# Performance work log

Hardware: AMD Instinct MI355X
Metric: run time of the kernel (lower is better)

The kernel has to match this reference:

```python
import jax, jax.numpy as jnp
import numpy as np

B, S, D, H = 1, 2048, 1024, 16
DH = D // H  # 64
ROPE_THETA = 10000.0


def _rope_tables(seq_len, half_dim, theta):
    inv = 1.0 / (theta ** (np.arange(0, half_dim, dtype=np.float32) / half_dim))
    ang = np.arange(seq_len, dtype=np.float32)[:, None] * inv[None, :]
    return jnp.asarray(np.cos(ang)), jnp.asarray(np.sin(ang))


def setup_inputs() -> dict:
    key = jax.random.key(0)
    ks = jax.random.split(key, 6)
    x = jax.random.normal(ks[0], (B, S, D), dtype=jnp.float32)
    # block-diagonal mask over ~4 packed images -> sorted segment ids
    seg_ids = jnp.sort(jax.random.randint(ks[1], (S,), 0, 4, dtype=jnp.int32))
    freqs_cos, freqs_sin = _rope_tables(S, DH // 2, ROPE_THETA)
    scale = 1.0 / np.sqrt(D)
    wq = jax.random.normal(ks[2], (D, D), dtype=jnp.float32) * scale
    wk = jax.random.normal(ks[3], (D, D), dtype=jnp.float32) * scale
    wv = jax.random.normal(ks[4], (D, D), dtype=jnp.float32) * scale
    wo = jax.random.normal(ks[5], (D, D), dtype=jnp.float32) * scale
    return {"x": x, "seg_ids": seg_ids, "freqs_cos": freqs_cos,
            "freqs_sin": freqs_sin, "wq": wq, "wk": wk, "wv": wv, "wo": wo}


def _apply_rope(t, cos, sin):
    # t: [B,S,H,DH]; interpret last dim as DH//2 complex pairs (real, imag)
    tr = t.reshape(B, S, H, DH // 2, 2)
    a, b = tr[..., 0], tr[..., 1]
    c = cos[None, :, None, :]  # [1,S,1,DH/2]
    s = sin[None, :, None, :]
    out = jnp.stack([a * c - b * s, a * s + b * c], axis=-1)
    return out.reshape(B, S, H, DH)


def reference(x, seg_ids, freqs_cos, freqs_sin, wq, wk, wv, wo):
    q = (x @ wq.T).reshape(B, S, H, DH)
    k = (x @ wk.T).reshape(B, S, H, DH)
    v = (x @ wv.T).reshape(B, S, H, DH)
    q = _apply_rope(q, freqs_cos, freqs_sin)
    k = _apply_rope(k, freqs_cos, freqs_sin)
    scores = jnp.einsum('bqhd,bkhd->bhqk', q, k) / np.float32(np.sqrt(DH))
    block_mask = (seg_ids[:, None] == seg_ids[None, :])  # [S,S] block-diagonal
    scores = jnp.where(block_mask[None, None], scores, jnp.float32(-1e9))
    attn = jax.nn.softmax(scores, axis=-1)
    out = jnp.einsum('bhqk,bkhd->bqhd', attn, v).reshape(B, S, D)
    return out @ wo.T
```

## Files before the change

### kernel.cpp

```cpp
#include <hip/hip_runtime.h>

typedef __bf16 bf16;
typedef __bf16 bf16x4 __attribute__((ext_vector_type(4)));
typedef __bf16 bf16x8 __attribute__((ext_vector_type(8)));
typedef float  f32x4  __attribute__((ext_vector_type(4)));

#define S_LEN 2048
#define D_DIM 1024
#define NHEAD 16
#define DHEAD 64

__device__ __forceinline__ void async_cp16(const bf16* g, bf16* l) {
  __builtin_amdgcn_global_load_lds(
      (__attribute__((address_space(1))) void*)(void*)g,
      (__attribute__((address_space(3))) void*)l,
      16, 0, 0);
}

__global__ __launch_bounds__(256) void cvt_k(
    const float* __restrict__ x,  const float* __restrict__ w0,
    const float* __restrict__ w1, const float* __restrict__ w2,
    const float* __restrict__ w3, bf16* __restrict__ dst,
    const int* __restrict__ seg, int* __restrict__ kbr)
{
  __shared__ int firstv[4];
  const int b = blockIdx.x;
  const int t = threadIdx.x;

  if (b < 3072) {
    int i = b * 256 + t;
    const float* src;
    int off;
    if (i < (1 << 18)) {
      src = x; off = i;
    } else {
      int j = i - (1 << 18);
      int s = j >> 17;
      off = j & ((1 << 17) - 1);
      src = (s == 0) ? w0 : (s == 1) ? w1 : (s == 2) ? w2 : w3;
    }
    f32x4 a = *(const f32x4*)(src + (size_t)off * 8);
    f32x4 bb = *(const f32x4*)(src + (size_t)off * 8 + 4);
    bf16x8 o;
    o[0] = (bf16)a[0];  o[1] = (bf16)a[1];  o[2] = (bf16)a[2];  o[3] = (bf16)a[3];
    o[4] = (bf16)bb[0]; o[5] = (bf16)bb[1]; o[6] = (bf16)bb[2]; o[7] = (bf16)bb[3];
    *((bf16x8*)dst + i) = o;
  } else {
    if (t < 4) firstv[t] = S_LEN;
    __syncthreads();
    for (int i = t; i < S_LEN; i += 256) {
      int s = seg[i];
      if (i == 0 || seg[i - 1] != s) atomicMin(&firstv[s], i);
    }
    __syncthreads();
    if (t < 32) {
      int smin = seg[t * 64], smax = seg[t * 64 + 63];
      int lb = S_LEN, ub = S_LEN;
      for (int vv = smin; vv < 4; ++vv) lb = min(lb, firstv[vv]);
      for (int vv = smax + 1; vv < 4; ++vv) ub = min(ub, firstv[vv]);
      kbr[t * 2] = lb >> 6;
      kbr[t * 2 + 1] = (ub - 1) >> 6;
    }
  }
}

__global__ __launch_bounds__(256) void gemm_qkv(
    const bf16* __restrict__ A,
    const bf16* __restrict__ B0, const bf16* __restrict__ B1,
    const bf16* __restrict__ B2,
    const float* __restrict__ cosT, const float* __restrict__ sinT,
    bf16* __restrict__ Cbase, bf16* __restrict__ Vt)
{
  constexpr int K = 1024, N = 1024;
  const int z = blockIdx.z;
  const bf16* W = (z == 0) ? B0 : (z == 1) ? B1 : B2;
  bf16* C = Cbase + (size_t)z * 2048 * 1024;

  __shared__ bf16 As0[128 * 32] __attribute__((aligned(16)));
  __shared__ bf16 As1[128 * 32] __attribute__((aligned(16)));
  __shared__ bf16 Bs0[64 * 32] __attribute__((aligned(16)));
  __shared__ bf16 Bs1[64 * 32] __attribute__((aligned(16)));

  const int t = threadIdx.x;
  const int lane = t & 63;
  const int w = t >> 6;
  const int lm = lane & 15, lq = lane >> 4;
  const int wr = w >> 1, wc = w & 1;
  const int bm = blockIdx.y, bn = blockIdx.x;

  const bf16* Abase = A + (size_t)bm * 128 * K;
  const bf16* Wbase = W + (size_t)bn * 64 * K;

  f32x4 acc[4][2] = {};

  for (int kk = 0; kk < K; kk += 64) {
#pragma unroll
    for (int g = 0; g < 2; ++g) {
      int c = (w * 2 + g) * 64 + lane;
      int row = c >> 2, k8 = c & 3;
      const bf16* ga = Abase + (size_t)row * K + kk + k8 * 8;
      async_cp16(ga, As0 + (w * 2 + g) * 512);
      async_cp16(ga + 32, As1 + (w * 2 + g) * 512);
    }
    {
      int c = w * 64 + lane;
      int row = c >> 2, k8 = c & 3;
      const bf16* gb = Wbase + (size_t)row * K + kk + k8 * 8;
      async_cp16(gb, Bs0 + w * 512);
      async_cp16(gb + 32, Bs1 + w * 512);
    }
    __syncthreads();

#pragma unroll
    for (int ks = 0; ks < 2; ++ks) {
      const bf16* As = ks ? As1 : As0;
      const bf16* Bs = ks ? Bs1 : Bs0;
      bf16x8 af[4], bfr[2];
#pragma unroll
      for (int mi = 0; mi < 4; ++mi)
        af[mi] = *(const bf16x8*)&As[(wr * 64 + mi * 16 + lm) * 32 + lq * 8];
#pragma unroll
      for (int ni = 0; ni < 2; ++ni)
        bfr[ni] = *(const bf16x8*)&Bs[(wc * 32 + ni * 16 + lm) * 32 + lq * 8];
#pragma unroll
      for (int mi = 0; mi < 4; ++mi)
#pragma unroll
        for (int ni = 0; ni < 2; ++ni)
          acc[mi][ni] = __builtin_amdgcn_mfma_f32_16x16x32_bf16(
              af[mi], bfr[ni], acc[mi][ni], 0, 0, 0);
    }
    __syncthreads();
  }

  if (z < 2) {
    const float scale = (z == 0) ? 0.125f : 1.0f;
#pragma unroll
    for (int mi = 0; mi < 4; ++mi)
#pragma unroll
      for (int ni = 0; ni < 2; ++ni) {
        int gcol = bn * 64 + wc * 32 + ni * 16 + lm;
        int p = (gcol & 63) >> 1;
        bool even = (gcol & 1) == 0;
#pragma unroll
        for (int r = 0; r < 4; ++r) {
          int row = bm * 128 + wr * 64 + mi * 16 + lq * 4 + r;
          float v = acc[mi][ni][r];
          float mate = __shfl_xor(v, 1);
          float cv = cosT[row * 32 + p];
          float sv = sinT[row * 32 + p];
          float res = even ? (v * cv - mate * sv) : (mate * sv + v * cv);
          C[(size_t)row * N + gcol] = (bf16)(res * scale);
        }
      }
  } else {
#pragma unroll
    for (int mi = 0; mi < 4; ++mi)
#pragma unroll
      for (int ni = 0; ni < 2; ++ni) {
        int gcol = bn * 64 + wc * 32 + ni * 16 + lm;
        int rowb = bm * 128 + wr * 64 + mi * 16 + lq * 4;
        bf16x4 pack;
#pragma unroll
        for (int r = 0; r < 4; ++r) pack[r] = (bf16)acc[mi][ni][r];
        *(bf16x4*)(Vt + (size_t)gcol * S_LEN + rowb) = pack;
      }
  }
}

__global__ __launch_bounds__(256) void gemm_wo(
    const bf16* __restrict__ A, const bf16* __restrict__ W,
    float* __restrict__ C)
{
  constexpr int K = 1024, N = 1024;

  __shared__ bf16 As0[64 * 32] __attribute__((aligned(16)));
  __shared__ bf16 As1[64 * 32] __attribute__((aligned(16)));
  __shared__ bf16 Bs0[64 * 32] __attribute__((aligned(16)));
  __shared__ bf16 Bs1[64 * 32] __attribute__((aligned(16)));

  const int t = threadIdx.x;
  const int lane = t & 63;
  const int w = t >> 6;
  const int lm = lane & 15, lq = lane >> 4;
  const int bn = blockIdx.x, bm = blockIdx.y;

  const bf16* Abase = A + (size_t)bm * 64 * K;
  const bf16* Wbase = W + (size_t)bn * 64 * K;

  f32x4 acc[4] = {};

  for (int kk = 0; kk < K; kk += 64) {
    {
      int c = w * 64 + lane;
      int row = c >> 2, k8 = c & 3;
      const bf16* ga = Abase + (size_t)row * K + kk + k8 * 8;
      async_cp16(ga, As0 + w * 512);
      async_cp16(ga + 32, As1 + w * 512);
      const bf16* gb = Wbase + (size_t)row * K + kk + k8 * 8;
      async_cp16(gb, Bs0 + w * 512);
      async_cp16(gb + 32, Bs1 + w * 512);
    }
    __syncthreads();

#pragma unroll
    for (int ks = 0; ks < 2; ++ks) {
      const bf16* As = ks ? As1 : As0;
      const bf16* Bs = ks ? Bs1 : Bs0;
      bf16x8 af = *(const bf16x8*)&As[(w * 16 + lm) * 32 + lq * 8];
      bf16x8 bfr[4];
#pragma unroll
      for (int ni = 0; ni < 4; ++ni)
        bfr[ni] = *(const bf16x8*)&Bs[(ni * 16 + lm) * 32 + lq * 8];
#pragma unroll
      for (int ni = 0; ni < 4; ++ni)
        acc[ni] = __builtin_amdgcn_mfma_f32_16x16x32_bf16(
            af, bfr[ni], acc[ni], 0, 0, 0);
    }
    __syncthreads();
  }

#pragma unroll
  for (int ni = 0; ni < 4; ++ni) {
    int col = bn * 64 + ni * 16 + lm;
#pragma unroll
    for (int r = 0; r < 4; ++r) {
      int row = bm * 64 + w * 16 + lq * 4 + r;
      C[(size_t)row * N + col] = acc[ni][r];
    }
  }
}

__global__ __launch_bounds__(256) void attn_k(
    const bf16* __restrict__ Q, const bf16* __restrict__ Kmat,
    const bf16* __restrict__ Vt, const int* __restrict__ seg,
    const int* __restrict__ kbr,
    float* __restrict__ Opar, float* __restrict__ Lpar)
{
  __shared__ bf16 Ks[64 * 72] __attribute__((aligned(16)));
  __shared__ bf16 Vs[64 * 72] __attribute__((aligned(16)));
  __shared__ bf16 Ps[4][16 * 72] __attribute__((aligned(16)));
  __shared__ int segk[64];

  const int h = blockIdx.y;
  const int qt = blockIdx.x & 31, par = blockIdx.x >> 5;
  const int q0 = qt * 64;
  const int t = threadIdx.x, lane = t & 63, w = t >> 6;
  const int lm = lane & 15, lq = lane >> 4;
  const int qrow = q0 + w * 16;

  const int kb0f = kbr[qt * 2], kb1f = kbr[qt * 2 + 1];

  bf16x8 qf[2];
#pragma unroll
  for (int ks = 0; ks < 2; ++ks)
    qf[ks] = *(const bf16x8*)(Q + (size_t)(qrow + lm) * D_DIM + h * DHEAD +
                              ks * 32 + lq * 8);

  int sq[4];
  float l_i[4];
#pragma unroll
  for (int r = 0; r < 4; ++r) {
    sq[r] = seg[qrow + lq * 4 + r];
    l_i[r] = 0.0f;
  }
  f32x4 o[4] = {};

  const int srow0 = t >> 3, sch = (t & 7) * 8;
  const int srow1 = (256 + t) >> 3;

  const int kbS = kb0f + par;
  f32x4 pk0, pk1, pv0, pv1;
  int psg;
  if (kbS <= kb1f) {
    const int k0 = kbS * 64;
    pk0 = *(const f32x4*)(Kmat + (size_t)(k0 + srow0) * D_DIM + h * DHEAD + sch);
    pk1 = *(const f32x4*)(Kmat + (size_t)(k0 + srow1) * D_DIM + h * DHEAD + sch);
    pv0 = *(const f32x4*)(Vt + (size_t)(h * DHEAD + srow0) * S_LEN + k0 + sch);
    pv1 = *(const f32x4*)(Vt + (size_t)(h * DHEAD + srow1) * S_LEN + k0 + sch);
    if (t < 64) psg = seg[k0 + t];
  }

  for (int kb = kbS; kb <= kb1f; kb += 2) {
    __syncthreads();
    *(f32x4*)&Ks[srow0 * 72 + sch] = pk0;
    *(f32x4*)&Ks[srow1 * 72 + sch] = pk1;
    *(f32x4*)&Vs[srow0 * 72 + sch] = pv0;
    *(f32x4*)&Vs[srow1 * 72 + sch] = pv1;
    if (t < 64) segk[t] = psg;
    __syncthreads();

    if (kb + 2 <= kb1f) {
      const int k0 = (kb + 2) * 64;
      pk0 = *(const f32x4*)(Kmat + (size_t)(k0 + srow0) * D_DIM + h * DHEAD + sch);
      pk1 = *(const f32x4*)(Kmat + (size_t)(k0 + srow1) * D_DIM + h * DHEAD + sch);
      pv0 = *(const f32x4*)(Vt + (size_t)(h * DHEAD + srow0) * S_LEN + k0 + sch);
      pv1 = *(const f32x4*)(Vt + (size_t)(h * DHEAD + srow1) * S_LEN + k0 + sch);
      if (t < 64) psg = seg[k0 + t];
    }

    f32x4 sa[4] = {};
#pragma unroll
    for (int ks = 0; ks < 2; ++ks) {
      bf16x8 kf[4];
#pragma unroll
      for (int ni = 0; ni < 4; ++ni)
        kf[ni] = *(const bf16x8*)&Ks[(ni * 16 + lm) * 72 + ks * 32 + lq * 8];
#pragma unroll
      for (int ni = 0; ni < 4; ++ni)
        sa[ni] = __builtin_amdgcn_mfma_f32_16x16x32_bf16(qf[ks], kf[ni],
                                                         sa[ni], 0, 0, 0);
    }

    int sk[4];
#pragma unroll
    for (int ni = 0; ni < 4; ++ni) sk[ni] = segk[ni * 16 + lm];

#pragma unroll
    for (int r = 0; r < 4; ++r)
#pragma unroll
      for (int ni = 0; ni < 4; ++ni) {
        float p = (sq[r] == sk[ni]) ? __expf(sa[ni][r]) : 0.0f;
        l_i[r] += p;
        Ps[w][(lq * 4 + r) * 72 + ni * 16 + lm] = (bf16)p;
      }

#pragma unroll
    for (int ks = 0; ks < 2; ++ks) {
      bf16x8 pf = *(const bf16x8*)&Ps[w][lm * 72 + ks * 32 + lq * 8];
      bf16x8 vf[4];
#pragma unroll
      for (int ni = 0; ni < 4; ++ni)
        vf[ni] = *(const bf16x8*)&Vs[(ni * 16 + lm) * 72 + ks * 32 + lq * 8];
#pragma unroll
      for (int ni = 0; ni < 4; ++ni)
        o[ni] = __builtin_amdgcn_mfma_f32_16x16x32_bf16(pf, vf[ni], o[ni],
                                                        0, 0, 0);
    }
  }

  float* Ob = Opar + ((size_t)(par * NHEAD + h) * S_LEN) * DHEAD;
  float* Lb = Lpar + (size_t)(par * NHEAD + h) * S_LEN;
#pragma unroll
  for (int r = 0; r < 4; ++r) {
    float l = l_i[r];
    l += __shfl_xor(l, 1);
    l += __shfl_xor(l, 2);
    l += __shfl_xor(l, 4);
    l += __shfl_xor(l, 8);
    int row = qrow + lq * 4 + r;
    if (lm == 0) Lb[row] = l;
#pragma unroll
    for (int ni = 0; ni < 4; ++ni)
      Ob[(size_t)row * DHEAD + ni * 16 + lm] = o[ni][r];
  }
}

__global__ __launch_bounds__(256) void combine_k(
    const float* __restrict__ Opar, const float* __restrict__ Lpar,
    bf16* __restrict__ AO)
{
  int idx = blockIdx.x * 256 + threadIdx.x;
  int c4 = idx & 15;
  int rh = idx >> 4;
  int row = rh & 2047;
  int h = rh >> 11;
  const size_t PO = (size_t)NHEAD * S_LEN * DHEAD;
  const float* o0 = Opar + ((size_t)h * S_LEN + row) * DHEAD + c4 * 4;
  f32x4 a = *(const f32x4*)o0;
  f32x4 b = *(const f32x4*)(o0 + PO);
  float l = Lpar[(size_t)h * S_LEN + row] +
            Lpar[(size_t)NHEAD * S_LEN + (size_t)h * S_LEN + row];
  float inv = 1.0f / l;
  bf16x4 ov;
#pragma unroll
  for (int j = 0; j < 4; ++j) ov[j] = (bf16)((a[j] + b[j]) * inv);
  *(bf16x4*)(AO + (size_t)row * D_DIM + h * DHEAD + c4 * 4) = ov;
}

extern "C" void kernel_launch(void* const* d_in, const int* in_sizes, int n_in,
                              void* d_out, int out_size, void* d_ws,
                              size_t ws_size, hipStream_t stream)
{
  const float* x  = (const float*)d_in[0];
  const int*   sg = (const int*)d_in[1];
  const float* fc = (const float*)d_in[2];
  const float* fs = (const float*)d_in[3];
  const float* wq = (const float*)d_in[4];
  const float* wk = (const float*)d_in[5];
  const float* wv = (const float*)d_in[6];
  const float* wo = (const float*)d_in[7];
  float* out = (float*)d_out;

  const size_t MAT = (size_t)S_LEN * D_DIM;
  const size_t WSZ = (size_t)D_DIM * D_DIM;
  bf16* xb  = (bf16*)d_ws;
  bf16* wqb = xb + MAT;
  bf16* wkb = wqb + WSZ;
  bf16* wvb = wkb + WSZ;
  bf16* wob = wvb + WSZ;
  bf16* q0  = wob + WSZ;
  bf16* k0  = q0 + MAT;
  bf16* vt  = k0 + MAT;
  bf16* ao  = vt + MAT;
  float* opar = (float*)(ao + MAT);
  float* lpar = opar + 2 * MAT;
  int*   kbr  = (int*)(lpar + 2 * NHEAD * S_LEN);

  dim3 blk(256);
  cvt_k<<<dim3(3073), blk, 0, stream>>>(x, wq, wk, wv, wo, xb, sg, kbr);
  gemm_qkv<<<dim3(16, 16, 3), blk, 0, stream>>>(xb, wqb, wkb, wvb, fc, fs,
                                                q0, vt);
  attn_k<<<dim3(64, 16), blk, 0, stream>>>(q0, k0, vt, sg, kbr, opar, lpar);
  combine_k<<<dim3(2048), blk, 0, stream>>>(opar, lpar, ao);
  gemm_wo<<<dim3(16, 32), blk, 0, stream>>>(ao, wob, out);
}
```

Baseline: 148.8 us.

## Fuse split-attention combine into output projection and register-prefetch GEMM tiles

Removes the separate combine kernel: the Wo GEMM now reads the two fp32 partial attention outputs and normalizers directly, sums them, normalizes and converts to bf16 while staging its A tile into LDS. Both GEMMs also replace direct global-to-LDS async copies with register-staged prefetch of the next K tile, issued after the LDS write so the loads overlap the MFMA work. This saves one launch and the bf16 round trip through global memory. In exchange the Wo GEMM reads fp32 partials redundantly across all 16 column blocks, which is more traffic, and register pressure goes up.

```diff
diff --git a/kernel.cpp b/kernel.cpp
--- a/kernel.cpp
+++ b/kernel.cpp
@@ -9,13 +9,6 @@
 #define D_DIM 1024
 #define NHEAD 16
 #define DHEAD 64
-
-__device__ __forceinline__ void async_cp16(const bf16* g, bf16* l) {
-  __builtin_amdgcn_global_load_lds(
-      (__attribute__((address_space(1))) void*)(void*)g,
-      (__attribute__((address_space(3))) void*)l,
-      16, 0, 0);
-}
 
 __global__ __launch_bounds__(256) void cvt_k(
     const float* __restrict__ x,  const float* __restrict__ w0,
@@ -88,28 +81,45 @@
   const int wr = w >> 1, wc = w & 1;
   const int bm = blockIdx.y, bn = blockIdx.x;
 
-  const bf16* Abase = A + (size_t)bm * 128 * K;
-  const bf16* Wbase = W + (size_t)bn * 64 * K;
+  const int arow = t >> 3;
+  const int half = (t & 7) >> 2, off = (t & 3) * 8;
+  const int koff = half * 32 + off;
+  bf16* const Adst = (half ? As1 : As0);
+  bf16* const Bdst = (half ? Bs1 : Bs0);
+
+  const bf16* Abase = A + (size_t)bm * 128 * K + koff;
+  const bf16* Wbase = W + (size_t)bn * 64 * K + koff;
+
+  bf16x8 ra[4], rb[2];
+#pragma unroll
+  for (int i = 0; i < 4; ++i)
+    ra[i] = *(const bf16x8*)(Abase + (size_t)(arow + 32 * i) * K);
+#pragma unroll
+  for (int i = 0; i < 2; ++i)
+    rb[i] = *(const bf16x8*)(Wbase + (size_t)(arow + 32 * i) * K);
 
   f32x4 acc[4][2] = {};
 
   for (int kk = 0; kk < K; kk += 64) {
-#pragma unroll
-    for (int g = 0; g < 2; ++g) {
-      int c = (w * 2 + g) * 64 + lane;
-      int row = c >> 2, k8 = c & 3;
-      const bf16* ga = Abase + (size_t)row * K + kk + k8 * 8;
-      async_cp16(ga, As0 + (w * 2 + g) * 512);
-      async_cp16(ga + 32, As1 + (w * 2 + g) * 512);
-    }
-    {
-      int c = w * 64 + lane;
-      int row = c >> 2, k8 = c & 3;
-      const bf16* gb = Wbase + (size_t)row * K + kk + k8 * 8;
-      async_cp16(gb, Bs0 + w * 512);
-      async_cp16(gb + 32, Bs1 + w * 512);
-    }
-    __syncthreads();
+    __syncthreads();
+#pragma unroll
+    for (int i = 0; i < 4; ++i)
+      *(bf16x8*)&Adst[(arow + 32 * i) * 32 + off] = ra[i];
+#pragma unroll
+    for (int i = 0; i < 2; ++i)
+      *(bf16x8*)&Bdst[(arow + 32 * i) * 32 + off] = rb[i];
+    __syncthreads();
+
+    if (kk + 64 < K) {
+      const bf16* An = Abase + kk + 64;
+      const bf16* Wn = Wbase + kk + 64;
+#pragma unroll
+      for (int i = 0; i < 4; ++i)
+        ra[i] = *(const bf16x8*)(An + (size_t)(arow + 32 * i) * K);
+#pragma unroll
+      for (int i = 0; i < 2; ++i)
+        rb[i] = *(const bf16x8*)(Wn + (size_t)(arow + 32 * i) * K);
+    }
 
 #pragma unroll
     for (int ks = 0; ks < 2; ++ks) {
@@ -129,7 +139,6 @@
           acc[mi][ni] = __builtin_amdgcn_mfma_f32_16x16x32_bf16(
               af[mi], bfr[ni], acc[mi][ni], 0, 0, 0);
     }
-    __syncthreads();
   }
 
   if (z < 2) {
@@ -168,8 +177,8 @@
 }
 
 __global__ __launch_bounds__(256) void gemm_wo(
-    const bf16* __restrict__ A, const bf16* __restrict__ W,
-    float* __restrict__ C)
+    const float* __restrict__ Opar, const float* __restrict__ Lpar,
+    const bf16* __restrict__ W, float* __restrict__ C)
 {
   constexpr int K = 1024, N = 1024;
 
@@ -184,23 +193,67 @@
   const int lm = lane & 15, lq = lane >> 4;
   const int bn = blockIdx.x, bm = blockIdx.y;
 
-  const bf16* Abase = A + (size_t)bm * 64 * K;
-  const bf16* Wbase = W + (size_t)bn * 64 * K;
+  const size_t PO = (size_t)NHEAD * S_LEN * DHEAD;
+  const size_t PL = (size_t)NHEAD * S_LEN;
+
+  const int arow = t >> 2, ak8 = (t & 3) * 8;
+  const int grow = bm * 64 + arow;
+  const int brow = t >> 3;
+  const int half = (t & 7) >> 2, off = (t & 3) * 8;
+  bf16* const Bdst = (half ? Bs1 : Bs0);
+  const bf16* Wbase = W + (size_t)bn * 64 * K + half * 32 + off;
+
+  f32x4 pa[2][4];
+  float il;
+  bf16x8 rb[2];
+
+  auto loadA = [&](int kk) {
+    int h = kk >> 6;
+    const float* b0 = Opar + ((size_t)h * S_LEN + grow) * DHEAD + ak8;
+#pragma unroll
+    for (int hh = 0; hh < 2; ++hh) {
+      pa[hh][0] = *(const f32x4*)(b0 + hh * 32);
+      pa[hh][1] = *(const f32x4*)(b0 + hh * 32 + 4);
+      pa[hh][2] = *(const f32x4*)(b0 + PO + hh * 32);
+      pa[hh][3] = *(const f32x4*)(b0 + PO + hh * 32 + 4);
+    }
+    float l0 = Lpar[(size_t)h * S_LEN + grow];
+    float l1 = Lpar[PL + (size_t)h * S_LEN + grow];
+    il = 1.0f / (l0 + l1);
+  };
+  auto loadB = [&](int kk) {
+#pragma unroll
+    for (int i = 0; i < 2; ++i)
+      rb[i] = *(const bf16x8*)(Wbase + (size_t)(brow + 32 * i) * K + kk);
+  };
+
+  loadA(0);
+  loadB(0);
 
   f32x4 acc[4] = {};
 
   for (int kk = 0; kk < K; kk += 64) {
-    {
-      int c = w * 64 + lane;
-      int row = c >> 2, k8 = c & 3;
-      const bf16* ga = Abase + (size_t)row * K + kk + k8 * 8;
-      async_cp16(ga, As0 + w * 512);
-      async_cp16(ga + 32, As1 + w * 512);
-      const bf16* gb = Wbase + (size_t)row * K + kk + k8 * 8;
-      async_cp16(gb, Bs0 + w * 512);
-      async_cp16(gb + 32, Bs1 + w * 512);
-    }
-    __syncthreads();
+    __syncthreads();
+#pragma unroll
+    for (int hh = 0; hh < 2; ++hh) {
+      bf16x8 av;
+#pragma unroll
+      for (int q = 0; q < 2; ++q) {
+        f32x4 s = pa[hh][q] + pa[hh][2 + q];
+#pragma unroll
+        for (int j = 0; j < 4; ++j) av[q * 4 + j] = (bf16)(s[j] * il);
+      }
+      *(bf16x8*)&(hh ? As1 : As0)[arow * 32 + ak8] = av;
+    }
+#pragma unroll
+    for (int i = 0; i < 2; ++i)
+      *(bf16x8*)&Bdst[(brow + 32 * i) * 32 + off] = rb[i];
+    __syncthreads();
+
+    if (kk + 64 < K) {
+      loadA(kk + 64);
+      loadB(kk + 64);
+    }
 
 #pragma unroll
     for (int ks = 0; ks < 2; ++ks) {
@@ -216,7 +269,6 @@
         acc[ni] = __builtin_amdgcn_mfma_f32_16x16x32_bf16(
             af, bfr[ni], acc[ni], 0, 0, 0);
     }
-    __syncthreads();
   }
 
 #pragma unroll
@@ -353,28 +405,6 @@
     for (int ni = 0; ni < 4; ++ni)
       Ob[(size_t)row * DHEAD + ni * 16 + lm] = o[ni][r];
   }
-}
-
-__global__ __launch_bounds__(256) void combine_k(
-    const float* __restrict__ Opar, const float* __restrict__ Lpar,
-    bf16* __restrict__ AO)
-{
-  int idx = blockIdx.x * 256 + threadIdx.x;
-  int c4 = idx & 15;
-  int rh = idx >> 4;
-  int row = rh & 2047;
-  int h = rh >> 11;
-  const size_t PO = (size_t)NHEAD * S_LEN * DHEAD;
-  const float* o0 = Opar + ((size_t)h * S_LEN + row) * DHEAD + c4 * 4;
-  f32x4 a = *(const f32x4*)o0;
-  f32x4 b = *(const f32x4*)(o0 + PO);
-  float l = Lpar[(size_t)h * S_LEN + row] +
-            Lpar[(size_t)NHEAD * S_LEN + (size_t)h * S_LEN + row];
-  float inv = 1.0f / l;
-  bf16x4 ov;
-#pragma unroll
-  for (int j = 0; j < 4; ++j) ov[j] = (bf16)((a[j] + b[j]) * inv);
-  *(bf16x4*)(AO + (size_t)row * D_DIM + h * DHEAD + c4 * 4) = ov;
 }
 
 extern "C" void kernel_launch(void* const* d_in, const int* in_sizes, int n_in,
@@ -401,8 +431,7 @@
   bf16* q0  = wob + WSZ;
   bf16* k0  = q0 + MAT;
   bf16* vt  = k0 + MAT;
-  bf16* ao  = vt + MAT;
-  float* opar = (float*)(ao + MAT);
+  float* opar = (float*)(vt + MAT);
   float* lpar = opar + 2 * MAT;
   int*   kbr  = (int*)(lpar + 2 * NHEAD * S_LEN);
 
@@ -411,6 +440,5 @@
   gemm_qkv<<<dim3(16, 16, 3), blk, 0, stream>>>(xb, wqb, wkb, wvb, fc, fs,
                                                 q0, vt);
   attn_k<<<dim3(64, 16), blk, 0, stream>>>(q0, k0, vt, sg, kbr, opar, lpar);
-  combine_k<<<dim3(2048), blk, 0, stream>>>(opar, lpar, ao);
-  gemm_wo<<<dim3(16, 32), blk, 0, stream>>>(ao, wob, out);
+  gemm_wo<<<dim3(16, 32), blk, 0, stream>>>(opar, lpar, wob, out);
 }
```

Result: slower. 155.3 us (+4.4%).

## Split attention KV range four ways and double GEMM k-step per barrier

Applied to the files above, without the earlier changes.

The attention kernel now splits each query tile's key range across four parallel blocks instead of two, doubling the grid, and the combine kernel sums four partial outputs and normalizers. Both GEMMs stage 128 k-elements per barrier instead of 64, halving the number of __syncthreads per tile at the cost of twice the shared memory. The aim is more parallelism in attention and less barrier overhead in the GEMMs. The cost is more partial-output traffic through global memory and lower occupancy from the larger shared buffers. The attention hunk only shows the stride change, so correct use of the partition index inside the kernel is assumed.

```diff
diff --git a/kernel.cpp b/kernel.cpp
--- a/kernel.cpp
+++ b/kernel.cpp
@@ -9,6 +9,7 @@
 #define D_DIM 1024
 #define NHEAD 16
 #define DHEAD 64
+#define NPAR 4
 
 __device__ __forceinline__ void async_cp16(const bf16* g, bf16* l) {
   __builtin_amdgcn_global_load_lds(
@@ -76,10 +77,8 @@
   const bf16* W = (z == 0) ? B0 : (z == 1) ? B1 : B2;
   bf16* C = Cbase + (size_t)z * 2048 * 1024;
 
-  __shared__ bf16 As0[128 * 32] __attribute__((aligned(16)));
-  __shared__ bf16 As1[128 * 32] __attribute__((aligned(16)));
-  __shared__ bf16 Bs0[64 * 32] __attribute__((aligned(16)));
-  __shared__ bf16 Bs1[64 * 32] __attribute__((aligned(16)));
+  __shared__ bf16 As[4][128 * 32] __attribute__((aligned(16)));
+  __shared__ bf16 Bs[4][64 * 32] __attribute__((aligned(16)));
 
   const int t = threadIdx.x;
   const int lane = t & 63;
@@ -93,35 +92,36 @@
 
   f32x4 acc[4][2] = {};
 
-  for (int kk = 0; kk < K; kk += 64) {
-#pragma unroll
-    for (int g = 0; g < 2; ++g) {
-      int c = (w * 2 + g) * 64 + lane;
-      int row = c >> 2, k8 = c & 3;
-      const bf16* ga = Abase + (size_t)row * K + kk + k8 * 8;
-      async_cp16(ga, As0 + (w * 2 + g) * 512);
-      async_cp16(ga + 32, As1 + (w * 2 + g) * 512);
-    }
-    {
+  for (int kk = 0; kk < K; kk += 128) {
+#pragma unroll
+    for (int kh = 0; kh < 2; ++kh)
+#pragma unroll
+      for (int g = 0; g < 2; ++g) {
+        int c = (w * 2 + g) * 64 + lane;
+        int row = c >> 2, k8 = c & 3;
+        const bf16* ga = Abase + (size_t)row * K + kk + kh * 64 + k8 * 8;
+        async_cp16(ga, &As[kh * 2][(w * 2 + g) * 512]);
+        async_cp16(ga + 32, &As[kh * 2 + 1][(w * 2 + g) * 512]);
+      }
+#pragma unroll
+    for (int kh = 0; kh < 2; ++kh) {
       int c = w * 64 + lane;
       int row = c >> 2, k8 = c & 3;
-      const bf16* gb = Wbase + (size_t)row * K + kk + k8 * 8;
-      async_cp16(gb, Bs0 + w * 512);
-      async_cp16(gb + 32, Bs1 + w * 512);
-    }
-    __syncthreads();
-
-#pragma unroll
-    for (int ks = 0; ks < 2; ++ks) {
-      const bf16* As = ks ? As1 : As0;
-      const bf16* Bs = ks ? Bs1 : Bs0;
+      const bf16* gb = Wbase + (size_t)row * K + kk + kh * 64 + k8 * 8;
+      async_cp16(gb, &Bs[kh * 2][w * 512]);
+      async_cp16(gb + 32, &Bs[kh * 2 + 1][w * 512]);
+    }
+    __syncthreads();
+
+#pragma unroll
+    for (int ks = 0; ks < 4; ++ks) {
       bf16x8 af[4], bfr[2];
 #pragma unroll
       for (int mi = 0; mi < 4; ++mi)
-        af[mi] = *(const bf16x8*)&As[(wr * 64 + mi * 16 + lm) * 32 + lq * 8];
+        af[mi] = *(const bf16x8*)&As[ks][(wr * 64 + mi * 16 + lm) * 32 + lq * 8];
 #pragma unroll
       for (int ni = 0; ni < 2; ++ni)
-        bfr[ni] = *(const bf16x8*)&Bs[(wc * 32 + ni * 16 + lm) * 32 + lq * 8];
+        bfr[ni] = *(const bf16x8*)&Bs[ks][(wc * 32 + ni * 16 + lm) * 32 + lq * 8];
 #pragma unroll
       for (int mi = 0; mi < 4; ++mi)
 #pragma unroll
@@ -173,10 +173,8 @@
 {
   constexpr int K = 1024, N = 1024;
 
-  __shared__ bf16 As0[64 * 32] __attribute__((aligned(16)));
-  __shared__ bf16 As1[64 * 32] __attribute__((aligned(16)));
-  __shared__ bf16 Bs0[64 * 32] __attribute__((aligned(16)));
-  __shared__ bf16 Bs1[64 * 32] __attribute__((aligned(16)));
+  __shared__ bf16 As[4][64 * 32] __attribute__((aligned(16)));
+  __shared__ bf16 Bs[4][64 * 32] __attribute__((aligned(16)));
 
   const int t = threadIdx.x;
   const int lane = t & 63;
@@ -189,28 +187,27 @@
 
   f32x4 acc[4] = {};
 
-  for (int kk = 0; kk < K; kk += 64) {
-    {
+  for (int kk = 0; kk < K; kk += 128) {
+#pragma unroll
+    for (int kh = 0; kh < 2; ++kh) {
       int c = w * 64 + lane;
       int row = c >> 2, k8 = c & 3;
-      const bf16* ga = Abase + (size_t)row * K + kk + k8 * 8;
-      async_cp16(ga, As0 + w * 512);
-      async_cp16(ga + 32, As1 + w * 512);
-      const bf16* gb = Wbase + (size_t)row * K + kk + k8 * 8;
-      async_cp16(gb, Bs0 + w * 512);
-      async_cp16(gb + 32, Bs1 + w * 512);
-    }
-    __syncthreads();
-
-#pragma unroll
-    for (int ks = 0; ks < 2; ++ks) {
-      const bf16* As = ks ? As1 : As0;
-      const bf16* Bs = ks ? Bs1 : Bs0;
-      bf16x8 af = *(const bf16x8*)&As[(w * 16 + lm) * 32 + lq * 8];
+      const bf16* ga = Abase + (size_t)row * K + kk + kh * 64 + k8 * 8;
+      async_cp16(ga, &As[kh * 2][w * 512]);
+      async_cp16(ga + 32, &As[kh * 2 + 1][w * 512]);
+      const bf16* gb = Wbase + (size_t)row * K + kk + kh * 64 + k8 * 8;
+      async_cp16(gb, &Bs[kh * 2][w * 512]);
+      async_cp16(gb + 32, &Bs[kh * 2 + 1][w * 512]);
+    }
+    __syncthreads();
+
+#pragma unroll
+    for (int ks = 0; ks < 4; ++ks) {
+      bf16x8 af = *(const bf16x8*)&As[ks][(w * 16 + lm) * 32 + lq * 8];
       bf16x8 bfr[4];
 #pragma unroll
       for (int ni = 0; ni < 4; ++ni)
-        bfr[ni] = *(const bf16x8*)&Bs[(ni * 16 + lm) * 32 + lq * 8];
+        bfr[ni] = *(const bf16x8*)&Bs[ks][(ni * 16 + lm) * 32 + lq * 8];
 #pragma unroll
       for (int ni = 0; ni < 4; ++ni)
         acc[ni] = __builtin_amdgcn_mfma_f32_16x16x32_bf16(
@@ -280,7 +277,7 @@
     if (t < 64) psg = seg[k0 + t];
   }
 
-  for (int kb = kbS; kb <= kb1f; kb += 2) {
+  for (int kb = kbS; kb <= kb1f; kb += NPAR) {
     __syncthreads();
     *(f32x4*)&Ks[srow0 * 72 + sch] = pk0;
     *(f32x4*)&Ks[srow1 * 72 + sch] = pk1;
@@ -289,8 +286,8 @@
     if (t < 64) segk[t] = psg;
     __syncthreads();
 
-    if (kb + 2 <= kb1f) {
-      const int k0 = (kb + 2) * 64;
+    if (kb + NPAR <= kb1f) {
+      const int k0 = (kb + NPAR) * 64;
       pk0 = *(const f32x4*)(Kmat + (size_t)(k0 + srow0) * D_DIM + h * DHEAD + sch);
       pk1 = *(const f32x4*)(Kmat + (size_t)(k0 + srow1) * D_DIM + h * DHEAD + sch);
       pv0 = *(const f32x4*)(Vt + (size_t)(h * DHEAD + srow0) * S_LEN + k0 + sch);
@@ -365,15 +362,19 @@
   int row = rh & 2047;
   int h = rh >> 11;
   const size_t PO = (size_t)NHEAD * S_LEN * DHEAD;
+  const size_t PL = (size_t)NHEAD * S_LEN;
   const float* o0 = Opar + ((size_t)h * S_LEN + row) * DHEAD + c4 * 4;
-  f32x4 a = *(const f32x4*)o0;
-  f32x4 b = *(const f32x4*)(o0 + PO);
-  float l = Lpar[(size_t)h * S_LEN + row] +
-            Lpar[(size_t)NHEAD * S_LEN + (size_t)h * S_LEN + row];
+  f32x4 s = {0.f, 0.f, 0.f, 0.f};
+  float l = 0.f;
+#pragma unroll
+  for (int p = 0; p < NPAR; ++p) {
+    s += *(const f32x4*)(o0 + p * PO);
+    l += Lpar[p * PL + (size_t)h * S_LEN + row];
+  }
   float inv = 1.0f / l;
   bf16x4 ov;
 #pragma unroll
-  for (int j = 0; j < 4; ++j) ov[j] = (bf16)((a[j] + b[j]) * inv);
+  for (int j = 0; j < 4; ++j) ov[j] = (bf16)(s[j] * inv);
   *(bf16x4*)(AO + (size_t)row * D_DIM + h * DHEAD + c4 * 4) = ov;
 }
 
@@ -403,14 +404,15 @@
   bf16* vt  = k0 + MAT;
   bf16* ao  = vt + MAT;
   float* opar = (float*)(ao + MAT);
-  float* lpar = opar + 2 * MAT;
-  int*   kbr  = (int*)(lpar + 2 * NHEAD * S_LEN);
+  float* lpar = opar + (size_t)NPAR * MAT;
+  int*   kbr  = (int*)(lpar + (size_t)NPAR * NHEAD * S_LEN);
 
   dim3 blk(256);
   cvt_k<<<dim3(3073), blk, 0, stream>>>(x, wq, wk, wv, wo, xb, sg, kbr);
   gemm_qkv<<<dim3(16, 16, 3), blk, 0, stream>>>(xb, wqb, wkb, wvb, fc, fs,
                                                 q0, vt);
-  attn_k<<<dim3(64, 16), blk, 0, stream>>>(q0, k0, vt, sg, kbr, opar, lpar);
+  attn_k<<<dim3(32 * NPAR, 16), blk, 0, stream>>>(q0, k0, vt, sg, kbr,
+                                                  opar, lpar);
   combine_k<<<dim3(2048), blk, 0, stream>>>(opar, lpar, ao);
   gemm_wo<<<dim3(16, 32), blk, 0, stream>>>(ao, wob, out);
 }
```

Result: no change. 147.3 us (-1.0%).
